# Optimization experiments

Measured on AMD Instinct MI355X. Metric: run time of the kernel, lower is better.

Reference implementation:

```python
import jax, jax.numpy as jnp
import numpy as np

EPS = 1e-6

def setup_inputs() -> dict:
    key = jax.random.key(0)
    k1, k2 = jax.random.split(key)
    pred_map = jax.random.uniform(k1, (64, 512, 512), dtype=jnp.float32)
    true_map = jax.random.uniform(k2, (64, 512, 512), dtype=jnp.float32)
    return {"pred_map": pred_map, "true_map": true_map}

def reference(pred_map, true_map):
    # per-sample normalize over all non-batch dims, then KL(true || pred), mean over batch
    B = pred_map.shape[0]
    pred = (pred_map + EPS).reshape(B, -1)
    true = (true_map + EPS).reshape(B, -1)
    pred = pred / jnp.sum(pred, axis=1, keepdims=True)
    true = true / jnp.sum(true, axis=1, keepdims=True)
    kl = jnp.sum(true * jnp.log(true / pred), axis=1)  # [B]
    return jnp.mean(kl)
```

## Files before the change

### kernel.cpp

```cpp
#include <hip/hip_runtime.h>
#include <hip/hip_bf16.h>

#define EPS 1e-6f

constexpr int B = 64;
constexpr int NPB = 512 * 512;
constexpr int BLOCKS_PER_BATCH = 32;
constexpr int NBLK = B * BLOCKS_PER_BATCH;
constexpr int THREADS = 256;
constexpr int CHUNK = NPB / BLOCKS_PER_BATCH;
constexpr int V4_PER_THREAD = CHUNK / 4 / THREADS;

__device__ __forceinline__ float waveReduce(float v) {
    #pragma unroll
    for (int off = 32; off > 0; off >>= 1) v += __shfl_down(v, off, 64);
    return v;
}

__global__ __launch_bounds__(THREADS) void kl_partial(
        const float* __restrict__ pred, const float* __restrict__ truem,
        float* __restrict__ ws) {
    const int b   = blockIdx.x / BLOCKS_PER_BATCH;
    const int blk = blockIdx.x % BLOCKS_PER_BATCH;
    const size_t base = (size_t)b * NPB + (size_t)blk * CHUNK;

    const float4* p4 = (const float4*)(pred + base);
    const float4* t4 = (const float4*)(truem + base);

    float4 pr[V4_PER_THREAD], tr[V4_PER_THREAD];
    #pragma unroll
    for (int j = 0; j < V4_PER_THREAD; ++j) pr[j] = p4[threadIdx.x + j * THREADS];
    #pragma unroll
    for (int j = 0; j < V4_PER_THREAD; ++j) tr[j] = t4[threadIdx.x + j * THREADS];

    __builtin_amdgcn_sched_barrier(0);

    float sp = 0.f, st = 0.f, s = 0.f;
    #pragma unroll
    for (int j = 0; j < V4_PER_THREAD; ++j) {
        float4 p = pr[j];
        float4 t = tr[j];
        sp += (p.x + p.y) + (p.z + p.w);
        st += (t.x + t.y) + (t.z + t.w);
        float px = p.x + EPS, py = p.y + EPS, pz = p.z + EPS, pw = p.w + EPS;
        float tx = t.x + EPS, ty = t.y + EPS, tz = t.z + EPS, tw = t.w + EPS;
        s += tx * (__logf(tx) - __logf(px));
        s += ty * (__logf(ty) - __logf(py));
        s += tz * (__logf(tz) - __logf(pz));
        s += tw * (__logf(tw) - __logf(pw));
    }

    sp = waveReduce(sp);
    st = waveReduce(st);
    s  = waveReduce(s);

    __shared__ float red[3][THREADS / 64];
    const int wave = threadIdx.x >> 6;
    const int lane = threadIdx.x & 63;
    if (lane == 0) { red[0][wave] = sp; red[1][wave] = st; red[2][wave] = s; }
    __syncthreads();
    if (threadIdx.x == 0) {
        float a0 = 0.f, a1 = 0.f, a2 = 0.f;
        #pragma unroll
        for (int w = 0; w < THREADS / 64; ++w) {
            a0 += red[0][w]; a1 += red[1][w]; a2 += red[2][w];
        }
        ws[blockIdx.x]            = a0;
        ws[NBLK + blockIdx.x]     = a1;
        ws[2 * NBLK + blockIdx.x] = a2;
    }
}

__global__ __launch_bounds__(64) void kl_final(
        const float* __restrict__ ws, float* __restrict__ out) {
    const int b = threadIdx.x;
    float Sp = 0.f, St = 0.f, S = 0.f;
    #pragma unroll
    for (int k = 0; k < BLOCKS_PER_BATCH; ++k) {
        const int idx = b * BLOCKS_PER_BATCH + k;
        Sp += ws[idx];
        St += ws[NBLK + idx];
        S  += ws[2 * NBLK + idx];
    }
    const float epsN = (float)NPB * EPS;
    Sp += epsN;
    St += epsN;
    float kl = S / St + logf(Sp / St);
    kl = waveReduce(kl);
    if (b == 0) out[0] = kl * (1.0f / B);
}

extern "C" void kernel_launch(void* const* d_in, const int* in_sizes, int n_in,
                              void* d_out, int out_size, void* d_ws, size_t ws_size,
                              hipStream_t stream) {
    const float* pred  = (const float*)d_in[0];
    const float* truem = (const float*)d_in[1];
    float* out = (float*)d_out;
    float* ws  = (float*)d_ws;

    kl_partial<<<NBLK, THREADS, 0, stream>>>(pred, truem, ws);
    kl_final<<<1, 64, 0, stream>>>(ws, out);
}
```

Measured before the change: 144.9 us.

## Stage inputs through LDS with direct global-to-LDS loads and smaller chunks

Replaces register-held vector loads with buffer loads that write straight into LDS (global_load_lds, 16 bytes per lane), then reads float4 values back from LDS for the log/KL math. The chunk per block drops from 8192 to 4096 elements, doubling the block count to 4096 and raising the workspace partial count. The aim is to cut register pressure and raise occupancy and memory-level parallelism. The cost is 32KB of LDS per block, an extra barrier and an LDS round trip. The final kernel's loop is now partially unrolled to handle the longer per-batch partial list.

```diff
diff --git a/kernel.cpp b/kernel.cpp
--- a/kernel.cpp
+++ b/kernel.cpp
@@ -5,11 +5,11 @@
 
 constexpr int B = 64;
 constexpr int NPB = 512 * 512;
-constexpr int BLOCKS_PER_BATCH = 32;
+constexpr int CHUNK = 4096;
+constexpr int BLOCKS_PER_BATCH = NPB / CHUNK;
 constexpr int NBLK = B * BLOCKS_PER_BATCH;
 constexpr int THREADS = 256;
-constexpr int CHUNK = NPB / BLOCKS_PER_BATCH;
-constexpr int V4_PER_THREAD = CHUNK / 4 / THREADS;
+constexpr int OPS_PER_WAVE = CHUNK / 256 / 4;
 
 __device__ __forceinline__ float waveReduce(float v) {
     #pragma unroll
@@ -17,29 +17,42 @@
     return v;
 }
 
+__device__ __forceinline__ void stage16(const float* g, float* l) {
+    __builtin_amdgcn_global_load_lds(
+        (const __attribute__((address_space(1))) void*)g,
+        (__attribute__((address_space(3))) void*)l, 16, 0, 0);
+}
+
 __global__ __launch_bounds__(THREADS) void kl_partial(
         const float* __restrict__ pred, const float* __restrict__ truem,
         float* __restrict__ ws) {
-    const int b   = blockIdx.x / BLOCKS_PER_BATCH;
-    const int blk = blockIdx.x % BLOCKS_PER_BATCH;
-    const size_t base = (size_t)b * NPB + (size_t)blk * CHUNK;
+    __shared__ float lds_p[CHUNK];
+    __shared__ float lds_t[CHUNK];
 
-    const float4* p4 = (const float4*)(pred + base);
-    const float4* t4 = (const float4*)(truem + base);
+    const size_t base = (size_t)blockIdx.x * CHUNK;
+    const int wave = threadIdx.x >> 6;
+    const int lane = threadIdx.x & 63;
 
-    float4 pr[V4_PER_THREAD], tr[V4_PER_THREAD];
     #pragma unroll
-    for (int j = 0; j < V4_PER_THREAD; ++j) pr[j] = p4[threadIdx.x + j * THREADS];
+    for (int j = 0; j < OPS_PER_WAVE; ++j) {
+        const int blkoff = (wave * OPS_PER_WAVE + j) * 256;
+        stage16(pred + base + blkoff + lane * 4, lds_p + blkoff);
+    }
     #pragma unroll
-    for (int j = 0; j < V4_PER_THREAD; ++j) tr[j] = t4[threadIdx.x + j * THREADS];
+    for (int j = 0; j < OPS_PER_WAVE; ++j) {
+        const int blkoff = (wave * OPS_PER_WAVE + j) * 256;
+        stage16(truem + base + blkoff + lane * 4, lds_t + blkoff);
+    }
+    __syncthreads();
 
-    __builtin_amdgcn_sched_barrier(0);
+    const float4* lp = (const float4*)lds_p;
+    const float4* lt = (const float4*)lds_t;
 
     float sp = 0.f, st = 0.f, s = 0.f;
     #pragma unroll
-    for (int j = 0; j < V4_PER_THREAD; ++j) {
-        float4 p = pr[j];
-        float4 t = tr[j];
+    for (int j = 0; j < CHUNK / 4 / THREADS; ++j) {
+        float4 p = lp[threadIdx.x + j * THREADS];
+        float4 t = lt[threadIdx.x + j * THREADS];
         sp += (p.x + p.y) + (p.z + p.w);
         st += (t.x + t.y) + (t.z + t.w);
         float px = p.x + EPS, py = p.y + EPS, pz = p.z + EPS, pw = p.w + EPS;
@@ -55,8 +68,6 @@
     s  = waveReduce(s);
 
     __shared__ float red[3][THREADS / 64];
-    const int wave = threadIdx.x >> 6;
-    const int lane = threadIdx.x & 63;
     if (lane == 0) { red[0][wave] = sp; red[1][wave] = st; red[2][wave] = s; }
     __syncthreads();
     if (threadIdx.x == 0) {
@@ -75,7 +86,7 @@
         const float* __restrict__ ws, float* __restrict__ out) {
     const int b = threadIdx.x;
     float Sp = 0.f, St = 0.f, S = 0.f;
-    #pragma unroll
+    #pragma unroll 8
     for (int k = 0; k < BLOCKS_PER_BATCH; ++k) {
         const int idx = b * BLOCKS_PER_BATCH + k;
         Sp += ws[idx];
```

Measured after the change: 143.0 us. No clear change (-1.3%).
